# Kernel optimization log

Hardware: AMD Instinct MI355X
Metric: run time of the kernel (lower is better)

## Reference

```python
import jax, jax.numpy as jnp
import numpy as np
from jax import lax

T = 2048          # tokens (batch*seq, module flattens to [-1, hidden])
H = 2048          # hidden_size
E = 32            # n_routed_experts
DF = 1024         # moe_intermediate_size
DS = 4096         # moe_shared_expert_intermediate_size
TOP_K = 6         # num_experts_per_tok
N_GROUP = 8
TOPK_GROUP = 4
SCALE = 2.5       # routed_scaling_factor
NORM_TOPK = True


def relu2(x):
    r = jax.nn.relu(x)
    return r * r


def setup_inputs() -> dict:
    key = jax.random.key(0)
    ks = jax.random.split(key, 7)
    s = 0.02
    return {
        "x": jax.random.normal(ks[0], (T, H), dtype=jnp.float32),
        "router_w": jax.random.normal(ks[1], (E, H), dtype=jnp.float32) * s,
        "router_b": jax.random.normal(ks[2], (E,), dtype=jnp.float32) * s,
        "w_up": jax.random.normal(ks[3], (E, H, DF), dtype=jnp.float32) * s,
        "w_down": jax.random.normal(ks[4], (E, DF, H), dtype=jnp.float32) * s,
        "shared_up": jax.random.normal(ks[5], (H, DS), dtype=jnp.float32) * s,
        "shared_down": jax.random.normal(ks[6], (DS, H), dtype=jnp.float32) * s,
    }


def _route(x, router_w, router_b):
    # router in fp32: logits -> sigmoid scores -> group-restricted top-k
    logits = x @ router_w.T                                  # [T, E]
    scores = jax.nn.sigmoid(logits)
    sfc = scores + router_b[None, :]                         # scores_for_choice
    gsize = E // N_GROUP
    grp = sfc.reshape(T, N_GROUP, gsize)
    group_scores = lax.top_k(grp, 2)[0].sum(-1)              # [T, n_group] sum of top-2
    _, gidx = lax.top_k(group_scores, TOPK_GROUP)            # [T, topk_group]
    group_mask = jax.nn.one_hot(gidx, N_GROUP, dtype=sfc.dtype).sum(1)  # [T, n_group]
    score_mask = jnp.repeat(group_mask, gsize, axis=1)       # [T, E]
    masked = jnp.where(score_mask > 0, sfc, 0.0)
    _, tidx = lax.top_k(masked, TOP_K)                       # [T, top_k]
    tw = jnp.take_along_axis(scores, tidx, axis=1)           # gather raw scores
    if NORM_TOPK:
        tw = tw / (tw.sum(-1, keepdims=True) + 1e-20)
    tw = tw * SCALE
    return tidx, tw


def reference(x, router_w, router_b, w_up, w_down, shared_up, shared_down):
    tidx, tw = _route(x, router_w, router_b)
    # dense combine weights [T, E]; equals sum of routed weights per expert
    combine = (jax.nn.one_hot(tidx, E, dtype=tw.dtype) * tw[..., None]).sum(1)
    # routed experts (no bias, so scaling before down_proj == scaling the output)
    h = jnp.einsum('td,edf->tef', x, w_up)                   # [T, E, DF]
    a = relu2(h) * combine[:, :, None]
    moe_out = jnp.einsum('tef,efd->td', a, w_down)           # [T, H]
    shared_out = relu2(x @ shared_up) @ shared_down
    return moe_out + shared_out
```

## Files before the change

### kernel.cpp

```cpp
#include <hip/hip_runtime.h>
#include <hip/hip_bf16.h>
#include <math.h>

#define T_TOK 2048
#define HID   2048
#define NE    32
#define DF    1024
#define DSZ   4096
#define TOPK  6
#define NGRP  8
#define TOPKG 4
#define RSCALE 2.5f
#define EXT_E 36
#define NSLOT 20480

typedef __attribute__((ext_vector_type(8))) short short8;
typedef __attribute__((ext_vector_type(4))) short short4v;
typedef __attribute__((ext_vector_type(4))) float f32x4;

typedef __attribute__((address_space(1))) const void gv1;
typedef __attribute__((address_space(3))) void lv3;

static __device__ __forceinline__ void gload16(const void* g, void* l) {
    __builtin_amdgcn_global_load_lds((gv1*)g, (lv3*)l, 16, 0, 0);
}

static __device__ __forceinline__ unsigned short f2b(float f) {
    union { float f; unsigned u; } v; v.f = f;
    unsigned r = v.u + 0x7fffu + ((v.u >> 16) & 1u);
    return (unsigned short)(r >> 16);
}

static __device__ __forceinline__ float b2f(unsigned short b) {
    union { float f; unsigned u; } v; v.u = ((unsigned)b) << 16;
    return v.f;
}

__global__ __launch_bounds__(256)
void router_kernel(const float* __restrict__ x, const float* __restrict__ rw,
                   const float* __restrict__ rb,
                   int* __restrict__ tidx, float* __restrict__ tw,
                   int* __restrict__ counts, unsigned short* __restrict__ xb) {
    __shared__ float xs[HID];
    __shared__ float part[256];
    __shared__ float scores[NE];
    __shared__ float sfc[NE];
    int t = blockIdx.x;
    int tid = threadIdx.x;
    for (int i = tid; i < HID / 4; i += 256) {
        ((float4*)xs)[i] = ((const float4*)(x + (size_t)t * HID))[i];
    }
    __syncthreads();
    {
        float4 a = ((const float4*)xs)[tid * 2];
        float4 b = ((const float4*)xs)[tid * 2 + 1];
        short8 o;
        o[0] = (short)f2b(a.x); o[1] = (short)f2b(a.y); o[2] = (short)f2b(a.z); o[3] = (short)f2b(a.w);
        o[4] = (short)f2b(b.x); o[5] = (short)f2b(b.y); o[6] = (short)f2b(b.z); o[7] = (short)f2b(b.w);
        *(short8*)(xb + (size_t)t * HID + tid * 8) = o;
    }
    int e = tid & 31, ch = tid >> 5;
    const float* w = rw + (size_t)e * HID + ch * 256;
    const float* xv = xs + ch * 256;
    float p = 0.f;
    #pragma unroll 8
    for (int k = 0; k < 256; ++k) p += xv[k] * w[k];
    part[tid] = p;
    __syncthreads();
    if (tid < 32) {
        float l = 0.f;
        #pragma unroll
        for (int c = 0; c < 8; ++c) l += part[c * 32 + tid];
        float s = 1.f / (1.f + expf(-l));
        scores[tid] = s;
        sfc[tid] = s + rb[tid];
    }
    __syncthreads();
    if (tid == 0) {
        float gs[NGRP];
        for (int g = 0; g < NGRP; ++g) {
            float v[4];
            for (int i = 0; i < 4; ++i) v[i] = sfc[g * 4 + i];
            int bi = 0;
            for (int i = 1; i < 4; ++i) if (v[i] > v[bi]) bi = i;
            float m1 = v[bi]; v[bi] = -INFINITY;
            int bj = 0;
            for (int i = 1; i < 4; ++i) if (v[i] > v[bj]) bj = i;
            gs[g] = m1 + v[bj];
        }
        bool gsel[NGRP];
        for (int g = 0; g < NGRP; ++g) gsel[g] = false;
        for (int k = 0; k < TOPKG; ++k) {
            int bi = -1; float b = -INFINITY;
            for (int g = 0; g < NGRP; ++g)
                if (!gsel[g] && gs[g] > b) { b = gs[g]; bi = g; }
            gsel[bi] = true;
        }
        float masked[NE];
        for (int i = 0; i < NE; ++i) masked[i] = gsel[i >> 2] ? sfc[i] : 0.0f;
        int sel[TOPK]; float wv[TOPK]; float wsum = 0.f;
        for (int k = 0; k < TOPK; ++k) {
            int bi = -1; float b = -INFINITY;
            for (int i = 0; i < NE; ++i)
                if (masked[i] > b) { b = masked[i]; bi = i; }
            masked[bi] = -INFINITY;
            sel[k] = bi; wv[k] = scores[bi]; wsum += wv[k];
        }
        float inv = RSCALE / (wsum + 1e-20f);
        for (int k = 0; k < TOPK; ++k) {
            tidx[t * TOPK + k] = sel[k];
            tw[t * TOPK + k] = wv[k] * inv;
            atomicAdd(&counts[sel[k]], 1);
        }
    }
}

__global__ void scan_kernel(const int* __restrict__ counts, int* __restrict__ offsets) {
    if (threadIdx.x == 0) {
        int a = 0;
        for (int e2 = 0; e2 < NE; ++e2) { offsets[e2] = a; a += counts[e2]; }
        offsets[NE] = a;
        for (int j = 1; j <= 4; ++j) offsets[NE + j] = 12288 + j * T_TOK;
    }
}

__global__ void scatter_kernel(const int* __restrict__ tidx, const float* __restrict__ tw,
                               const int* __restrict__ offsets, int* __restrict__ cursors,
                               int* __restrict__ perm, float* __restrict__ pw,
                               int* __restrict__ slot_of) {
    int t = blockIdx.x * blockDim.x + threadIdx.x;
    if (t >= T_TOK) return;
    for (int k = 0; k < TOPK; ++k) {
        int e = tidx[t * TOPK + k];
        int pos = atomicAdd(&cursors[e], 1);
        int slot = offsets[e] + pos;
        perm[slot] = t;
        pw[slot] = tw[t * TOPK + k];
        slot_of[t * TOPK + k] = slot;
    }
    #pragma unroll
    for (int j = 0; j < 4; ++j) {
        int slot = 12288 + j * T_TOK + t;
        perm[slot] = t;
        pw[slot] = 1.0f;
    }
}

__global__ __launch_bounds__(256)
void cvt_weights_kernel(const float* __restrict__ w_up, const float* __restrict__ w_dn,
                        const float* __restrict__ sh_up, const float* __restrict__ sh_dn,
                        unsigned short* __restrict__ wupb, unsigned short* __restrict__ wdnb,
                        unsigned short* __restrict__ shupb, unsigned short* __restrict__ shdnb) {
    size_t c = (size_t)blockIdx.x * 256 + threadIdx.x;
    const float* src; unsigned short* dst; size_t off;
    if (c < 8388608ull)        { src = w_up;  dst = wupb;  off = c; }
    else if (c < 16777216ull)  { src = w_dn;  dst = wdnb;  off = c - 8388608ull; }
    else if (c < 17825792ull)  { src = sh_up; dst = shupb; off = c - 16777216ull; }
    else                       { src = sh_dn; dst = shdnb; off = c - 17825792ull; }
    float4 a = ((const float4*)src)[off * 2];
    float4 b = ((const float4*)src)[off * 2 + 1];
    short8 o;
    o[0] = (short)f2b(a.x); o[1] = (short)f2b(a.y); o[2] = (short)f2b(a.z); o[3] = (short)f2b(a.w);
    o[4] = (short)f2b(b.x); o[5] = (short)f2b(b.y); o[6] = (short)f2b(b.z); o[7] = (short)f2b(b.w);
    *(short8*)(dst + off * 8) = o;
}

template<int MODE>
__global__ __launch_bounds__(256, 2)
void gemm_tr_kernel(const unsigned short* __restrict__ Abuf,
                    const unsigned short* __restrict__ Wmain, const unsigned short* __restrict__ Wsh,
                    unsigned short* __restrict__ Cbuf, const int* __restrict__ offsets,
                    const int* __restrict__ perm, const float* __restrict__ pw) {
    constexpr int K = (MODE == 0) ? HID : DF;
    constexpr int N = (MODE == 0) ? DF : HID;
    __shared__ __align__(16) char lds[32768];
    char* As = lds;
    char* Bs = lds + 16384;

    int tid = threadIdx.x;
    int lane = tid & 63, wvid = tid >> 6, wr = wvid >> 1, wc = wvid & 1;

    int bz = blockIdx.z;
    int off = offsets[bz], end = offsets[bz + 1];
    int row0 = off + blockIdx.y * 128;
    if (row0 >= end) return;
    int n0 = blockIdx.x * 128;

    const unsigned short* Bsrc; long ldbb;
    if (MODE == 0) {
        if (bz < NE) { Bsrc = Wmain + (size_t)bz * HID * DF; ldbb = DF; }
        else         { Bsrc = Wsh + (size_t)(bz - NE) * DF;  ldbb = DSZ; }
    } else {
        Bsrc = (bz < NE) ? (Wmain + (size_t)bz * DF * HID)
                         : (Wsh + (size_t)(bz - NE) * DF * HID);
        ldbb = HID;
    }

    int lr = lane >> 3;
    int csrc = (((lane & 7) ^ lr) << 4);
    size_t abyte[4];
    int ldsA[4];
    #pragma unroll
    for (int p = 0; p < 4; ++p) {
        int r = p * 32 + wvid * 8 + lr;
        int gr = row0 + r;
        if (gr > end - 1) gr = end - 1;
        int s = (MODE == 0) ? perm[gr] : gr;
        abyte[p] = (size_t)s * (K * 2);
        ldsA[p] = (p * 32 + wvid * 8) * 128;
    }

    int bk = (lane >> 1) & 3;
    int bn = (lane >> 3) * 16 + (lane & 1) * 8;
    size_t bbyte[4];
    int ldsB[4];
    #pragma unroll
    for (int p = 0; p < 4; ++p) {
        int kg = wvid + 4 * p;
        bbyte[p] = ((size_t)(kg * 4 + bk) * ldbb + n0 + bn) * 2;
        ldsB[p] = kg * 1024;
    }

    unsigned bsb = (unsigned)(uintptr_t)(lv3*)Bs + (unsigned)((lane >> 4) * 2048 + (lane & 15) * 8);

    f32x4 acc[4][4] = {};
    for (int k0 = 0; k0 < K; k0 += 64) {
        size_t kbB = (size_t)k0 * (ldbb * 2);
        __syncthreads();
        #pragma unroll
        for (int p = 0; p < 4; ++p) {
            gload16((const char*)Abuf + abyte[p] + k0 * 2 + csrc, As + ldsA[p]);
            gload16((const char*)Bsrc + kbB + bbyte[p], Bs + ldsB[p]);
        }
        __syncthreads();
        #pragma unroll
        for (int ks = 0; ks < 2; ++ks) {
            int r16 = lane & 15, kg = lane >> 4;
            short8 af[4];
            #pragma unroll
            for (int m = 0; m < 4; ++m) {
                int r = wr * 64 + m * 16 + r16;
                af[m] = *(const short8*)(As + r * 128 + ((ks * 64 + kg * 16) ^ ((r & 7) << 4)));
            }
            short4v t0[4], t1[4];
            #pragma unroll
            for (int n = 0; n < 4; ++n) {
                unsigned a = bsb + ks * 8192 + (wc * 4 + n) * 128;
                asm volatile("ds_read_b64_tr_b16 %0, %2\n\t"
                             "ds_read_b64_tr_b16 %1, %2 offset:1024"
                             : "=v"(t0[n]), "=v"(t1[n]) : "v"(a));
            }
            asm volatile("s_waitcnt lgkmcnt(0)" ::: "memory");
            __builtin_amdgcn_sched_barrier(0);
            #pragma unroll
            for (int n = 0; n < 4; ++n) {
                short8 bfr;
                bfr[0] = t0[n][0]; bfr[1] = t0[n][1]; bfr[2] = t0[n][2]; bfr[3] = t0[n][3];
                bfr[4] = t1[n][0]; bfr[5] = t1[n][1]; bfr[6] = t1[n][2]; bfr[7] = t1[n][3];
                #pragma unroll
                for (int m = 0; m < 4; ++m)
                    acc[m][n] = __builtin_amdgcn_mfma_f32_16x16x32_bf16(af[m], bfr, acc[m][n], 0, 0, 0);
            }
        }
    }

    int r16 = lane & 15, rg = lane >> 4;
    #pragma unroll
    for (int m = 0; m < 4; ++m) {
        #pragma unroll
        for (int j = 0; j < 4; ++j) {
            int rr = row0 + wr * 64 + m * 16 + rg * 4 + j;
            if (rr < end) {
                if (MODE == 0) {
                    float scale = pw[rr];
                    #pragma unroll
                    for (int n = 0; n < 4; ++n) {
                        int cc = n0 + wc * 64 + n * 16 + r16;
                        float v = acc[m][n][j];
                        v = v > 0.f ? v * v : 0.f;
                        Cbuf[(size_t)rr * N + cc] = f2b(v * scale);
                    }
                } else {
                    #pragma unroll
                    for (int n = 0; n < 4; ++n) {
                        int cc = n0 + wc * 64 + n * 16 + r16;
                        Cbuf[(size_t)rr * N + cc] = f2b(acc[m][n][j]);
                    }
                }
            }
        }
    }
}

__global__ void combine_kernel(const unsigned short* __restrict__ slotout,
                               const int* __restrict__ slot_of,
                               float* __restrict__ out) {
    int t = blockIdx.x, tid = threadIdx.x;
    int s[10];
    #pragma unroll
    for (int k = 0; k < TOPK; ++k) s[k] = slot_of[t * TOPK + k];
    #pragma unroll
    for (int j = 0; j < 4; ++j) s[TOPK + j] = 12288 + j * T_TOK + t;
    int c = tid * 8;
    float a[8] = {0.f, 0.f, 0.f, 0.f, 0.f, 0.f, 0.f, 0.f};
    #pragma unroll
    for (int k = 0; k < 10; ++k) {
        short8 v = *(const short8*)(slotout + (size_t)s[k] * HID + c);
        #pragma unroll
        for (int i = 0; i < 8; ++i) a[i] += b2f((unsigned short)v[i]);
    }
    *(float4*)(out + (size_t)t * HID + c) = make_float4(a[0], a[1], a[2], a[3]);
    *(float4*)(out + (size_t)t * HID + c + 4) = make_float4(a[4], a[5], a[6], a[7]);
}

extern "C" void kernel_launch(void* const* d_in, const int* in_sizes, int n_in,
                              void* d_out, int out_size, void* d_ws, size_t ws_size,
                              hipStream_t stream) {
    const float* x     = (const float*)d_in[0];
    const float* rw    = (const float*)d_in[1];
    const float* rb    = (const float*)d_in[2];
    const float* w_up  = (const float*)d_in[3];
    const float* w_dn  = (const float*)d_in[4];
    const float* sh_up = (const float*)d_in[5];
    const float* sh_dn = (const float*)d_in[6];
    float* out = (float*)d_out;
    char* ws = (char*)d_ws;

    int*   counts  = (int*)(ws);
    int*   cursors = (int*)(ws + 128);
    int*   offsets = (int*)(ws + 256);
    int*   tidx    = (int*)(ws + 1024);
    float* tw      = (float*)(ws + 50176);
    int*   slot_of = (int*)(ws + 99328);
    int*   perm    = (int*)(ws + 148480);
    float* pw      = (float*)(ws + 230400);
    unsigned short* xb      = (unsigned short*)(ws + 312320);
    unsigned short* act     = (unsigned short*)(ws + 8700928);
    unsigned short* slotout = (unsigned short*)(ws + 50643968);
    unsigned short* wupb    = (unsigned short*)(ws + 134530048);
    unsigned short* wdnb    = (unsigned short*)(ws + 268747776);
    unsigned short* shupb   = (unsigned short*)(ws + 402965504);
    unsigned short* shdnb   = (unsigned short*)(ws + 419742720);

    hipMemsetAsync(ws, 0, 256, stream);

    router_kernel<<<T_TOK, 256, 0, stream>>>(x, rw, rb, tidx, tw, counts, xb);
    scan_kernel<<<1, 64, 0, stream>>>(counts, offsets);
    scatter_kernel<<<(T_TOK + 255) / 256, 256, 0, stream>>>(tidx, tw, offsets, cursors,
                                                            perm, pw, slot_of);

    cvt_weights_kernel<<<73728, 256, 0, stream>>>(w_up, w_dn, sh_up, sh_dn,
                                                  wupb, wdnb, shupb, shdnb);

    gemm_tr_kernel<0><<<dim3(DF / 128, T_TOK / 128, EXT_E), 256, 0, stream>>>(
        xb, wupb, shupb, act, offsets, perm, pw);

    gemm_tr_kernel<1><<<dim3(HID / 128, T_TOK / 128, EXT_E), 256, 0, stream>>>(
        act, wdnb, shdnb, slotout, offsets, perm, pw);

    combine_kernel<<<T_TOK, 256, 0, stream>>>(slotout, slot_of, out);
}
```

Baseline: 596.7 us.

## Overlap weight bf16 conversion with router and up-projection GEMM kernels

Removes the standalone weight-conversion kernel. The up-weight conversion is folded into the router launch, with router blocks interleaved every tenth block. The down-weight conversion is folded into the up-projection GEMM launch, with GEMM tiles interleaved every fifth block. The aim is to hide memory-bound conversion behind compute and cut launch serialization, at the cost of heterogeneous blocks competing for occupancy and LDS, since conversion blocks inherit the GEMM launch bounds.

```diff
diff --git a/kernel.cpp b/kernel.cpp
--- a/kernel.cpp
+++ b/kernel.cpp
@@ -36,16 +36,24 @@
     return v.f;
 }
 
-__global__ __launch_bounds__(256)
-void router_kernel(const float* __restrict__ x, const float* __restrict__ rw,
-                   const float* __restrict__ rb,
-                   int* __restrict__ tidx, float* __restrict__ tw,
-                   int* __restrict__ counts, unsigned short* __restrict__ xb) {
+static __device__ __forceinline__ void cvt_chunk(const float* __restrict__ src,
+                                                 unsigned short* __restrict__ dst, size_t off) {
+    float4 a = ((const float4*)src)[off * 2];
+    float4 b = ((const float4*)src)[off * 2 + 1];
+    short8 o;
+    o[0] = (short)f2b(a.x); o[1] = (short)f2b(a.y); o[2] = (short)f2b(a.z); o[3] = (short)f2b(a.w);
+    o[4] = (short)f2b(b.x); o[5] = (short)f2b(b.y); o[6] = (short)f2b(b.z); o[7] = (short)f2b(b.w);
+    *(short8*)(dst + off * 8) = o;
+}
+
+static __device__ void router_body(int t, const float* __restrict__ x,
+                                   const float* __restrict__ rw, const float* __restrict__ rb,
+                                   int* __restrict__ tidx, float* __restrict__ tw,
+                                   int* __restrict__ counts, unsigned short* __restrict__ xb) {
     __shared__ float xs[HID];
     __shared__ float part[256];
     __shared__ float scores[NE];
     __shared__ float sfc[NE];
-    int t = blockIdx.x;
     int tid = threadIdx.x;
     for (int i = tid; i < HID / 4; i += 256) {
         ((float4*)xs)[i] = ((const float4*)(x + (size_t)t * HID))[i];
@@ -112,6 +120,27 @@
             tw[t * TOPK + k] = wv[k] * inv;
             atomicAdd(&counts[sel[k]], 1);
         }
+    }
+}
+
+__global__ __launch_bounds__(256)
+void router_cvtup_kernel(const float* __restrict__ x, const float* __restrict__ rw,
+                         const float* __restrict__ rb,
+                         int* __restrict__ tidx, float* __restrict__ tw,
+                         int* __restrict__ counts, unsigned short* __restrict__ xb,
+                         const float* __restrict__ w_up, const float* __restrict__ sh_up,
+                         unsigned short* __restrict__ wupb, unsigned short* __restrict__ shupb) {
+    int bid = blockIdx.x;
+    if (bid % 10 == 0) {
+        router_body(bid / 10, x, rw, rb, tidx, tw, counts, xb);
+        return;
+    }
+    size_t base = (size_t)(bid - bid / 10 - 1) * 256 + threadIdx.x;
+    #pragma unroll
+    for (int i = 0; i < 2; ++i) {
+        size_t c = base + (size_t)i * 4718592ull;
+        if (c < 8388608ull) cvt_chunk(w_up, wupb, c);
+        else                cvt_chunk(sh_up, shupb, c - 8388608ull);
     }
 }
 
@@ -146,31 +175,14 @@
     }
 }
 
-__global__ __launch_bounds__(256)
-void cvt_weights_kernel(const float* __restrict__ w_up, const float* __restrict__ w_dn,
-                        const float* __restrict__ sh_up, const float* __restrict__ sh_dn,
-                        unsigned short* __restrict__ wupb, unsigned short* __restrict__ wdnb,
-                        unsigned short* __restrict__ shupb, unsigned short* __restrict__ shdnb) {
-    size_t c = (size_t)blockIdx.x * 256 + threadIdx.x;
-    const float* src; unsigned short* dst; size_t off;
-    if (c < 8388608ull)        { src = w_up;  dst = wupb;  off = c; }
-    else if (c < 16777216ull)  { src = w_dn;  dst = wdnb;  off = c - 8388608ull; }
-    else if (c < 17825792ull)  { src = sh_up; dst = shupb; off = c - 16777216ull; }
-    else                       { src = sh_dn; dst = shdnb; off = c - 17825792ull; }
-    float4 a = ((const float4*)src)[off * 2];
-    float4 b = ((const float4*)src)[off * 2 + 1];
-    short8 o;
-    o[0] = (short)f2b(a.x); o[1] = (short)f2b(a.y); o[2] = (short)f2b(a.z); o[3] = (short)f2b(a.w);
-    o[4] = (short)f2b(b.x); o[5] = (short)f2b(b.y); o[6] = (short)f2b(b.z); o[7] = (short)f2b(b.w);
-    *(short8*)(dst + off * 8) = o;
-}
-
 template<int MODE>
-__global__ __launch_bounds__(256, 2)
-void gemm_tr_kernel(const unsigned short* __restrict__ Abuf,
-                    const unsigned short* __restrict__ Wmain, const unsigned short* __restrict__ Wsh,
-                    unsigned short* __restrict__ Cbuf, const int* __restrict__ offsets,
-                    const int* __restrict__ perm, const float* __restrict__ pw) {
+static __device__ void gemm_body(int bx, int by, int bz,
+                                 const unsigned short* __restrict__ Abuf,
+                                 const unsigned short* __restrict__ Wmain,
+                                 const unsigned short* __restrict__ Wsh,
+                                 unsigned short* __restrict__ Cbuf,
+                                 const int* __restrict__ offsets,
+                                 const int* __restrict__ perm, const float* __restrict__ pw) {
     constexpr int K = (MODE == 0) ? HID : DF;
     constexpr int N = (MODE == 0) ? DF : HID;
     __shared__ __align__(16) char lds[32768];
@@ -180,11 +192,10 @@
     int tid = threadIdx.x;
     int lane = tid & 63, wvid = tid >> 6, wr = wvid >> 1, wc = wvid & 1;
 
-    int bz = blockIdx.z;
     int off = offsets[bz], end = offsets[bz + 1];
-    int row0 = off + blockIdx.y * 128;
+    int row0 = off + by * 128;
     if (row0 >= end) return;
-    int n0 = blockIdx.x * 128;
+    int n0 = bx * 128;
 
     const unsigned short* Bsrc; long ldbb;
     if (MODE == 0) {
@@ -292,6 +303,40 @@
     }
 }
 
+__global__ __launch_bounds__(256, 2)
+void gemm_up_cvtdn_kernel(const unsigned short* __restrict__ xb,
+                          const unsigned short* __restrict__ wupb,
+                          const unsigned short* __restrict__ shupb,
+                          unsigned short* __restrict__ act,
+                          const int* __restrict__ offsets, const int* __restrict__ perm,
+                          const float* __restrict__ pw,
+                          const float* __restrict__ w_dn, const float* __restrict__ sh_dn,
+                          unsigned short* __restrict__ wdnb, unsigned short* __restrict__ shdnb) {
+    int bid = blockIdx.x;
+    if (bid % 5 != 0) {
+        size_t base = (size_t)(bid - bid / 5 - 1) * 256 + threadIdx.x;
+        #pragma unroll
+        for (int i = 0; i < 2; ++i) {
+            size_t c = base + (size_t)i * 4718592ull;
+            if (c < 8388608ull) cvt_chunk(w_dn, wdnb, c);
+            else                cvt_chunk(sh_dn, shdnb, c - 8388608ull);
+        }
+        return;
+    }
+    int g = bid / 5;
+    gemm_body<0>(g & 7, (g >> 3) & 15, g >> 7, xb, wupb, shupb, act, offsets, perm, pw);
+}
+
+__global__ __launch_bounds__(256, 2)
+void gemm_down_kernel(const unsigned short* __restrict__ act,
+                      const unsigned short* __restrict__ wdnb,
+                      const unsigned short* __restrict__ shdnb,
+                      unsigned short* __restrict__ slotout,
+                      const int* __restrict__ offsets, const float* __restrict__ pw) {
+    gemm_body<1>(blockIdx.x, blockIdx.y, blockIdx.z, act, wdnb, shdnb, slotout,
+                 offsets, nullptr, pw);
+}
+
 __global__ void combine_kernel(const unsigned short* __restrict__ slotout,
                                const int* __restrict__ slot_of,
                                float* __restrict__ out) {
@@ -344,19 +389,17 @@
 
     hipMemsetAsync(ws, 0, 256, stream);
 
-    router_kernel<<<T_TOK, 256, 0, stream>>>(x, rw, rb, tidx, tw, counts, xb);
+    router_cvtup_kernel<<<20480, 256, 0, stream>>>(x, rw, rb, tidx, tw, counts, xb,
+                                                   w_up, sh_up, wupb, shupb);
     scan_kernel<<<1, 64, 0, stream>>>(counts, offsets);
     scatter_kernel<<<(T_TOK + 255) / 256, 256, 0, stream>>>(tidx, tw, offsets, cursors,
                                                             perm, pw, slot_of);
 
-    cvt_weights_kernel<<<73728, 256, 0, stream>>>(w_up, w_dn, sh_up, sh_dn,
-                                                  wupb, wdnb, shupb, shdnb);
-
-    gemm_tr_kernel<0><<<dim3(DF / 128, T_TOK / 128, EXT_E), 256, 0, stream>>>(
-        xb, wupb, shupb, act, offsets, perm, pw);
-
-    gemm_tr_kernel<1><<<dim3(HID / 128, T_TOK / 128, EXT_E), 256, 0, stream>>>(
-        act, wdnb, shdnb, slotout, offsets, perm, pw);
+    gemm_up_cvtdn_kernel<<<23040, 256, 0, stream>>>(xb, wupb, shupb, act, offsets, perm, pw,
+                                                    w_dn, sh_dn, wdnb, shdnb);
+
+    gemm_down_kernel<<<dim3(HID / 128, T_TOK / 128, EXT_E), 256, 0, stream>>>(
+        act, wdnb, shdnb, slotout, offsets, pw);
 
     combine_kernel<<<T_TOK, 256, 0, stream>>>(slotout, slot_of, out);
 }
```

Result: slower. 627.9 us (+5.2%).
